# Performance work log

Measured on AMD Instinct MI355X. Metric: run time of the kernel, lower is better.

The kernel has to match this reference:

```python
import jax, jax.numpy as jnp
import numpy as np

COS_EPS = 1e-8  # torch F.cosine_similarity eps


def setup_inputs() -> dict:
    key = jax.random.key(0)
    k1, k2 = jax.random.split(key)
    x = jax.random.normal(k1, (8192, 512), dtype=jnp.float32)
    class_logits = jax.random.normal(k2, (8192, 100), dtype=jnp.float32)
    return {"x": x, "class_logits": class_logits}


def reference(x, class_logits):
    N, D = x.shape
    C = class_logits.shape[1]

    # class_logits.clone().detach()
    logits = jax.lax.stop_gradient(class_logits)
    pred = jax.nn.softmax(logits, axis=1)
    max_logit = pred.max(axis=1)          # [N]
    max_cls = pred.argmax(axis=1)         # [N] int

    # graph(): pairwise cosine similarity = normalize rows + gram matmul
    norms = jnp.linalg.norm(x, axis=1, keepdims=True)
    xn = x / jnp.maximum(norms, COS_EPS)
    mat = xn @ xn.T                       # [N, N]

    x_agg = mat @ x + x                   # [N, D]
    x_new = jax.lax.stop_gradient(x_agg)

    # update_prototype: per-class weighted scatter-add then mean over counts
    weighted = x_new * max_logit[:, None]                     # [N, D]
    sums = jax.ops.segment_sum(weighted, max_cls, num_segments=C)      # [C, D]
    counts = jax.ops.segment_sum(jnp.ones((N,), x.dtype), max_cls, num_segments=C)  # [C]
    prototypes = jnp.where(counts[:, None] > 0,
                           sums / jnp.maximum(counts, 1.0)[:, None],
                           jnp.zeros_like(sums))              # [C, D]

    # inter_class_matrix[i, j] = prototypes[j] - prototypes[i]
    inter_class_matrix = prototypes[None, :, :] - prototypes[:, None, :]  # [C, C, D]
    return prototypes, inter_class_matrix
```

## Files before the change

### kernel.cpp

```cpp
#include <hip/hip_runtime.h>
#include <math.h>

#define N_ROWS 8192
#define D_DIM  512
#define C_CLS  100

typedef unsigned short u16;
typedef __attribute__((ext_vector_type(8))) short short8;
typedef __attribute__((ext_vector_type(4))) float floatx4;

#define WS_G      0
#define WS_SUMS   262144
#define WS_COUNTS 313344
#define WS_INV    313472
#define WS_WV     321664
#define WS_CLS    329856
#define WS_GH     338048
#define WS_GL     469120
#define WS_XH     600192
#define WS_XL     2697344
#define WS_XTH    4794496
#define WS_XTL    6891648
#define WS_NTH    8988800
#define WS_NTL    11085952
#define WS_ZERO_FLOATS 313472

__device__ __forceinline__ void split2(float v, u16& h, u16& l) {
    unsigned u = __float_as_uint(v);
    h = (u16)(u >> 16);
    float r = v - __uint_as_float(u & 0xFFFF0000u);
    l = (u16)(__float_as_uint(r) >> 16);
}

__global__ void k_softmax(const float* __restrict__ logits,
                          float* __restrict__ wv, int* __restrict__ cls,
                          float* __restrict__ counts) {
    int wave = (blockIdx.x * blockDim.x + threadIdx.x) >> 6;
    int lane = threadIdx.x & 63;
    if (wave >= N_ROWS) return;
    const float* row = logits + (size_t)wave * C_CLS;
    float v1 = row[lane];
    bool has2 = (lane + 64) < C_CLS;
    float v2 = has2 ? row[lane + 64] : -INFINITY;
    float m; int idx;
    if (v2 > v1) { m = v2; idx = lane + 64; } else { m = v1; idx = lane; }
    #pragma unroll
    for (int off = 32; off >= 1; off >>= 1) {
        float om = __shfl_down(m, off);
        int   oi = __shfl_down(idx, off);
        if (om > m || (om == m && oi < idx)) { m = om; idx = oi; }
    }
    m = __shfl(m, 0);
    idx = __shfl(idx, 0);
    float s = expf(v1 - m) + (has2 ? expf(v2 - m) : 0.0f);
    #pragma unroll
    for (int off = 32; off >= 1; off >>= 1) s += __shfl_down(s, off);
    if (lane == 0) {
        wv[wave] = 1.0f / s;
        cls[wave] = idx;
        atomicAdd(&counts[idx], 1.0f);
    }
}

__global__ void k_norm(const float* __restrict__ x, float* __restrict__ inv) {
    int wave = (blockIdx.x * blockDim.x + threadIdx.x) >> 6;
    int lane = threadIdx.x & 63;
    if (wave >= N_ROWS) return;
    const float* row = x + (size_t)wave * D_DIM;
    float ss = 0.f;
    #pragma unroll
    for (int j = 0; j < D_DIM; j += 64) {
        float v = row[j + lane];
        ss += v * v;
    }
    #pragma unroll
    for (int off = 32; off >= 1; off >>= 1) ss += __shfl_down(ss, off);
    if (lane == 0) inv[wave] = 1.0f / fmaxf(sqrtf(ss), 1e-8f);
}

#define LDT 65
__global__ __launch_bounds__(256) void k_convert(const float* __restrict__ x,
        const float* __restrict__ inv,
        u16* __restrict__ xh, u16* __restrict__ xl,
        u16* __restrict__ xth, u16* __restrict__ xtl,
        u16* __restrict__ nth, u16* __restrict__ ntl) {
    __shared__ unsigned xt_p[64 * LDT];
    __shared__ unsigned nt_p[64 * LDT];
    int r0 = blockIdx.x * 64, c0 = blockIdx.y * 64;
    int t = threadIdx.x;
    int r = t >> 2, cq = t & 3;
    const float* src = x + (size_t)(r0 + r) * D_DIM + c0 + cq * 16;
    float vv[16];
    {
        float4 a = *(const float4*)(src + 0);
        float4 b = *(const float4*)(src + 4);
        float4 c = *(const float4*)(src + 8);
        float4 d = *(const float4*)(src + 12);
        vv[0]=a.x; vv[1]=a.y; vv[2]=a.z; vv[3]=a.w;
        vv[4]=b.x; vv[5]=b.y; vv[6]=b.z; vv[7]=b.w;
        vv[8]=c.x; vv[9]=c.y; vv[10]=c.z; vv[11]=c.w;
        vv[12]=d.x; vv[13]=d.y; vv[14]=d.z; vv[15]=d.w;
    }
    float iv = inv[r0 + r];
    u16 hh[16], ll[16];
    #pragma unroll
    for (int j = 0; j < 16; ++j) {
        split2(vv[j], hh[j], ll[j]);
        u16 nh, nl;
        split2(iv * vv[j], nh, nl);
        int cl = cq * 16 + j;
        xt_p[cl * LDT + r] = ((unsigned)hh[j] << 16) | ll[j];
        nt_p[cl * LDT + r] = ((unsigned)nh   << 16) | nl;
    }
    {
        size_t base = (size_t)(r0 + r) * D_DIM + c0 + cq * 16;
        uint oh[8], ol[8];
        #pragma unroll
        for (int p = 0; p < 8; ++p) {
            oh[p] = (unsigned)hh[2*p] | ((unsigned)hh[2*p+1] << 16);
            ol[p] = (unsigned)ll[2*p] | ((unsigned)ll[2*p+1] << 16);
        }
        *(uint4*)&xh[base]     = make_uint4(oh[0], oh[1], oh[2], oh[3]);
        *(uint4*)&xh[base + 8] = make_uint4(oh[4], oh[5], oh[6], oh[7]);
        *(uint4*)&xl[base]     = make_uint4(ol[0], ol[1], ol[2], ol[3]);
        *(uint4*)&xl[base + 8] = make_uint4(ol[4], ol[5], ol[6], ol[7]);
    }
    __syncthreads();
    int c = t >> 2, rq = (t & 3) * 16;
    size_t tbase = (size_t)(c0 + c) * N_ROWS + r0 + rq;
    {
        uint oh[8], ol[8];
        #pragma unroll
        for (int p = 0; p < 8; ++p) {
            unsigned d0 = xt_p[c * LDT + rq + 2*p];
            unsigned d1 = xt_p[c * LDT + rq + 2*p + 1];
            oh[p] = (d0 >> 16) | (d1 & 0xFFFF0000u);
            ol[p] = (d0 & 0xFFFFu) | (d1 << 16);
        }
        *(uint4*)&xth[tbase]     = make_uint4(oh[0], oh[1], oh[2], oh[3]);
        *(uint4*)&xth[tbase + 8] = make_uint4(oh[4], oh[5], oh[6], oh[7]);
        *(uint4*)&xtl[tbase]     = make_uint4(ol[0], ol[1], ol[2], ol[3]);
        *(uint4*)&xtl[tbase + 8] = make_uint4(ol[4], ol[5], ol[6], ol[7]);
    }
    {
        uint oh[8], ol[8];
        #pragma unroll
        for (int p = 0; p < 8; ++p) {
            unsigned d0 = nt_p[c * LDT + rq + 2*p];
            unsigned d1 = nt_p[c * LDT + rq + 2*p + 1];
            oh[p] = (d0 >> 16) | (d1 & 0xFFFF0000u);
            ol[p] = (d0 & 0xFFFFu) | (d1 << 16);
        }
        *(uint4*)&nth[tbase]     = make_uint4(oh[0], oh[1], oh[2], oh[3]);
        *(uint4*)&nth[tbase + 8] = make_uint4(oh[4], oh[5], oh[6], oh[7]);
        *(uint4*)&ntl[tbase]     = make_uint4(ol[0], ol[1], ol[2], ol[3]);
        *(uint4*)&ntl[tbase + 8] = make_uint4(ol[4], ol[5], ol[6], ol[7]);
    }
}

#define STR 40
__global__ __launch_bounds__(256) void k_gemm1(const u16* __restrict__ nth,
        const u16* __restrict__ ntl, const u16* __restrict__ xth,
        const u16* __restrict__ xtl, float* __restrict__ G) {
    __shared__ u16 Ah[64 * STR], Al[64 * STR], Bh[64 * STR], Bl[64 * STR];
    int i0 = (blockIdx.x & 7) * 64, j0 = (blockIdx.x >> 3) * 64;
    int kb = blockIdx.y * (N_ROWS / 8);
    int t = threadIdx.x, w = t >> 6, l = t & 63;
    int sr = t >> 2, sc = (t & 3) * 8;
    floatx4 acc[4];
    floatx4 zero = {0.f, 0.f, 0.f, 0.f};
    #pragma unroll
    for (int nn = 0; nn < 4; ++nn) acc[nn] = zero;
    for (int s = 0; s < 32; ++s) {
        int ks = kb + s * 32 + sc;
        *(uint4*)&Ah[sr * STR + sc] = *(const uint4*)&nth[(size_t)(i0 + sr) * N_ROWS + ks];
        *(uint4*)&Al[sr * STR + sc] = *(const uint4*)&ntl[(size_t)(i0 + sr) * N_ROWS + ks];
        *(uint4*)&Bh[sr * STR + sc] = *(const uint4*)&xth[(size_t)(j0 + sr) * N_ROWS + ks];
        *(uint4*)&Bl[sr * STR + sc] = *(const uint4*)&xtl[(size_t)(j0 + sr) * N_ROWS + ks];
        __syncthreads();
        int ar = (w * 16 + (l & 15)) * STR + (l >> 4) * 8;
        short8 a_h = *(const short8*)&Ah[ar];
        short8 a_l = *(const short8*)&Al[ar];
        #pragma unroll
        for (int nn = 0; nn < 4; ++nn) {
            int br = (nn * 16 + (l & 15)) * STR + (l >> 4) * 8;
            short8 b_h = *(const short8*)&Bh[br];
            short8 b_l = *(const short8*)&Bl[br];
            acc[nn] = __builtin_amdgcn_mfma_f32_16x16x32_bf16(a_h, b_h, acc[nn], 0, 0, 0);
            acc[nn] = __builtin_amdgcn_mfma_f32_16x16x32_bf16(a_h, b_l, acc[nn], 0, 0, 0);
            acc[nn] = __builtin_amdgcn_mfma_f32_16x16x32_bf16(a_l, b_h, acc[nn], 0, 0, 0);
        }
        __syncthreads();
    }
    int row0 = i0 + w * 16 + (l >> 4) * 4;
    int col0 = j0 + (l & 15);
    #pragma unroll
    for (int nn = 0; nn < 4; ++nn)
        #pragma unroll
        for (int r = 0; r < 4; ++r)
            atomicAdd(&G[(size_t)(row0 + r) * D_DIM + col0 + nn * 16], acc[nn][r]);
}

__global__ void k_split(const float* __restrict__ G, u16* __restrict__ Gh,
                        u16* __restrict__ Gl) {
    int i = blockIdx.x * 256 + threadIdx.x;
    u16 h, l;
    split2(G[i], h, l);
    Gh[i] = h; Gl[i] = l;
}

__global__ __launch_bounds__(256) void k_gemm2(const u16* __restrict__ xh,
        const u16* __restrict__ xl, const u16* __restrict__ Gh,
        const u16* __restrict__ Gl, const float* __restrict__ x,
        const float* __restrict__ inv, const float* __restrict__ wv,
        const int* __restrict__ cls, float* __restrict__ sums) {
    __shared__ u16 Xh[128 * STR], Xl[128 * STR], Bh2[64 * STR], Bl2[64 * STR];
    int m0 = blockIdx.x * 128, j0 = blockIdx.y * 64;
    int t = threadIdx.x, w = t >> 6, l = t & 63;
    int sr = t >> 2, sc = (t & 3) * 8;
    floatx4 acc[2][4];
    floatx4 zero = {0.f, 0.f, 0.f, 0.f};
    #pragma unroll
    for (int mi = 0; mi < 2; ++mi)
        #pragma unroll
        for (int nn = 0; nn < 4; ++nn) acc[mi][nn] = zero;
    for (int s = 0; s < 16; ++s) {
        int ks = s * 32 + sc;
        *(uint4*)&Xh[sr * STR + sc]        = *(const uint4*)&xh[(size_t)(m0 + sr) * D_DIM + ks];
        *(uint4*)&Xh[(64 + sr) * STR + sc] = *(const uint4*)&xh[(size_t)(m0 + 64 + sr) * D_DIM + ks];
        *(uint4*)&Xl[sr * STR + sc]        = *(const uint4*)&xl[(size_t)(m0 + sr) * D_DIM + ks];
        *(uint4*)&Xl[(64 + sr) * STR + sc] = *(const uint4*)&xl[(size_t)(m0 + 64 + sr) * D_DIM + ks];
        *(uint4*)&Bh2[sr * STR + sc]       = *(const uint4*)&Gh[(size_t)(j0 + sr) * D_DIM + ks];
        *(uint4*)&Bl2[sr * STR + sc]       = *(const uint4*)&Gl[(size_t)(j0 + sr) * D_DIM + ks];
        __syncthreads();
        int ar0 = (w * 32 + (l & 15)) * STR + (l >> 4) * 8;
        int ar1 = (w * 32 + 16 + (l & 15)) * STR + (l >> 4) * 8;
        short8 ah0 = *(const short8*)&Xh[ar0];
        short8 al0 = *(const short8*)&Xl[ar0];
        short8 ah1 = *(const short8*)&Xh[ar1];
        short8 al1 = *(const short8*)&Xl[ar1];
        #pragma unroll
        for (int nn = 0; nn < 4; ++nn) {
            int br = (nn * 16 + (l & 15)) * STR + (l >> 4) * 8;
            short8 b_h = *(const short8*)&Bh2[br];
            short8 b_l = *(const short8*)&Bl2[br];
            acc[0][nn] = __builtin_amdgcn_mfma_f32_16x16x32_bf16(ah0, b_h, acc[0][nn], 0, 0, 0);
            acc[0][nn] = __builtin_amdgcn_mfma_f32_16x16x32_bf16(ah0, b_l, acc[0][nn], 0, 0, 0);
            acc[0][nn] = __builtin_amdgcn_mfma_f32_16x16x32_bf16(al0, b_h, acc[0][nn], 0, 0, 0);
            acc[1][nn] = __builtin_amdgcn_mfma_f32_16x16x32_bf16(ah1, b_h, acc[1][nn], 0, 0, 0);
            acc[1][nn] = __builtin_amdgcn_mfma_f32_16x16x32_bf16(ah1, b_l, acc[1][nn], 0, 0, 0);
            acc[1][nn] = __builtin_amdgcn_mfma_f32_16x16x32_bf16(al1, b_h, acc[1][nn], 0, 0, 0);
        }
        __syncthreads();
    }
    int col = j0 + (l & 15);
    #pragma unroll
    for (int mi = 0; mi < 2; ++mi) {
        int rb = m0 + w * 32 + mi * 16 + (l >> 4) * 4;
        #pragma unroll
        for (int r = 0; r < 4; ++r) {
            int m = rb + r;
            float ivm = inv[m], wm = wv[m];
            int cm = cls[m];
            #pragma unroll
            for (int nn = 0; nn < 4; ++nn) {
                int d = col + nn * 16;
                float y = ivm * acc[mi][nn][r] + x[(size_t)m * D_DIM + d];
                atomicAdd(&sums[(size_t)cm * D_DIM + d], wm * y);
            }
        }
    }
}

__global__ void k_proto(const float* __restrict__ sums,
                        const float* __restrict__ counts,
                        float* __restrict__ out) {
    int i = blockIdx.x * blockDim.x + threadIdx.x;
    if (i >= C_CLS * D_DIM) return;
    int c = i >> 9;
    float cnt = counts[c];
    out[i] = (cnt > 0.f) ? sums[i] / fmaxf(cnt, 1.f) : 0.f;
}

__global__ void k_inter(const float* __restrict__ proto, float* __restrict__ out) {
    int pair = blockIdx.x;
    int i = pair / C_CLS;
    int j = pair - i * C_CLS;
    int d = threadIdx.x << 2;
    float4 pj = *(const float4*)&proto[j * D_DIM + d];
    float4 pi = *(const float4*)&proto[i * D_DIM + d];
    float4 r;
    r.x = pj.x - pi.x; r.y = pj.y - pi.y; r.z = pj.z - pi.z; r.w = pj.w - pi.w;
    *(float4*)&out[(size_t)pair * D_DIM + d] = r;
}

extern "C" void kernel_launch(void* const* d_in, const int* in_sizes, int n_in,
                              void* d_out, int out_size, void* d_ws, size_t ws_size,
                              hipStream_t stream) {
    const float* x      = (const float*)d_in[0];
    const float* logits = (const float*)d_in[1];
    float* out = (float*)d_out;
    float* ws  = (float*)d_ws;
    float* G      = ws + WS_G;
    float* sums   = ws + WS_SUMS;
    float* counts = ws + WS_COUNTS;
    float* inv    = ws + WS_INV;
    float* wv     = ws + WS_WV;
    int*   cls    = (int*)(ws + WS_CLS);
    u16* Gh  = (u16*)(ws + WS_GH);
    u16* Gl  = (u16*)(ws + WS_GL);
    u16* xh  = (u16*)(ws + WS_XH);
    u16* xl  = (u16*)(ws + WS_XL);
    u16* xth = (u16*)(ws + WS_XTH);
    u16* xtl = (u16*)(ws + WS_XTL);
    u16* nth = (u16*)(ws + WS_NTH);
    u16* ntl = (u16*)(ws + WS_NTL);

    hipMemsetAsync(d_ws, 0, WS_ZERO_FLOATS * sizeof(float), stream);
    k_softmax<<<N_ROWS / 4, 256, 0, stream>>>(logits, wv, cls, counts);
    k_norm<<<N_ROWS / 4, 256, 0, stream>>>(x, inv);
    k_convert<<<dim3(128, 8), 256, 0, stream>>>(x, inv, xh, xl, xth, xtl, nth, ntl);
    k_gemm1<<<dim3(64, 8), 256, 0, stream>>>(nth, ntl, xth, xtl, G);
    k_split<<<D_DIM * D_DIM / 256, 256, 0, stream>>>(G, Gh, Gl);
    k_gemm2<<<dim3(64, 8), 256, 0, stream>>>(xh, xl, Gh, Gl, x, inv, wv, cls, sums);
    k_proto<<<(C_CLS * D_DIM + 255) / 256, 256, 0, stream>>>(sums, counts, out);
    k_inter<<<C_CLS * C_CLS, 128, 0, stream>>>(out, out + C_CLS * D_DIM);
}
```

Baseline: 195.6 us.

## Reassociate prototype computation to per-class reductions times Gram matrix, drop second GEMM

The N×D by D×D second GEMM and its atomic scatter are replaced by an algebraic reassociation. Rows are bucketed by class through a count, scan and scatter pass. Each class then reduces its weighted rows into two D-vectors and multiplies one of them by the D×D Gram matrix G in fp32. The first GEMM now uses 128x128 tiles with global_load_lds direct copies and writes 32 K-split partials, which a separate kernel reduces instead of using float atomics. This removes the large second GEMM, the x split buffers and the G split step. In exchange it adds extra small kernels, a 32 MB partial buffer, and a per-class loop whose length depends on how many rows land in each class.

```diff
diff --git a/kernel.cpp b/kernel.cpp
--- a/kernel.cpp
+++ b/kernel.cpp
@@ -6,24 +6,23 @@
 #define C_CLS  100
 
 typedef unsigned short u16;
+typedef unsigned int u32;
 typedef __attribute__((ext_vector_type(8))) short short8;
 typedef __attribute__((ext_vector_type(4))) float floatx4;
 
 #define WS_G      0
-#define WS_SUMS   262144
-#define WS_COUNTS 313344
-#define WS_INV    313472
-#define WS_WV     321664
-#define WS_CLS    329856
-#define WS_GH     338048
-#define WS_GL     469120
-#define WS_XH     600192
-#define WS_XL     2697344
-#define WS_XTH    4794496
-#define WS_XTL    6891648
-#define WS_NTH    8988800
-#define WS_NTL    11085952
-#define WS_ZERO_FLOATS 313472
+#define WS_GP     262144
+#define WS_INV    8650752
+#define WS_WV     8658944
+#define WS_CLS    8667136
+#define WS_CNT    8675328
+#define WS_OFFS   8675456
+#define WS_CUR    8675584
+#define WS_ORDER  8675712
+#define WS_NTH    8683904
+#define WS_NTL    10781056
+#define WS_XTH    12878208
+#define WS_XTL    14975360
 
 __device__ __forceinline__ void split2(float v, u16& h, u16& l) {
     unsigned u = __float_as_uint(v);
@@ -32,9 +31,15 @@
     l = (u16)(__float_as_uint(r) >> 16);
 }
 
+typedef const __attribute__((address_space(1))) u32* gp32;
+typedef __attribute__((address_space(3))) u32* lp32;
+__device__ __forceinline__ void cp16(const u16* g, u16* l) {
+    __builtin_amdgcn_global_load_lds((gp32)g, (lp32)l, 16, 0, 0);
+}
+
 __global__ void k_softmax(const float* __restrict__ logits,
                           float* __restrict__ wv, int* __restrict__ cls,
-                          float* __restrict__ counts) {
+                          int* __restrict__ cnt) {
     int wave = (blockIdx.x * blockDim.x + threadIdx.x) >> 6;
     int lane = threadIdx.x & 63;
     if (wave >= N_ROWS) return;
@@ -58,7 +63,7 @@
     if (lane == 0) {
         wv[wave] = 1.0f / s;
         cls[wave] = idx;
-        atomicAdd(&counts[idx], 1.0f);
+        atomicAdd(&cnt[idx], 1);
     }
 }
 
@@ -78,10 +83,24 @@
     if (lane == 0) inv[wave] = 1.0f / fmaxf(sqrtf(ss), 1e-8f);
 }
 
+__global__ void k_scan(const int* __restrict__ cnt, int* __restrict__ offs) {
+    if (threadIdx.x == 0) {
+        int acc = 0;
+        for (int c = 0; c < C_CLS; ++c) { offs[c] = acc; acc += cnt[c]; }
+    }
+}
+
+__global__ void k_scatter(const int* __restrict__ cls, const int* __restrict__ offs,
+                          int* __restrict__ cursor, int* __restrict__ order) {
+    int m = blockIdx.x * 256 + threadIdx.x;
+    int c = cls[m];
+    int pos = atomicAdd(&cursor[c], 1);
+    order[offs[c] + pos] = m;
+}
+
 #define LDT 65
 __global__ __launch_bounds__(256) void k_convert(const float* __restrict__ x,
         const float* __restrict__ inv,
-        u16* __restrict__ xh, u16* __restrict__ xl,
         u16* __restrict__ xth, u16* __restrict__ xtl,
         u16* __restrict__ nth, u16* __restrict__ ntl) {
     __shared__ unsigned xt_p[64 * LDT];
@@ -102,28 +121,14 @@
         vv[12]=d.x; vv[13]=d.y; vv[14]=d.z; vv[15]=d.w;
     }
     float iv = inv[r0 + r];
-    u16 hh[16], ll[16];
     #pragma unroll
     for (int j = 0; j < 16; ++j) {
-        split2(vv[j], hh[j], ll[j]);
-        u16 nh, nl;
+        u16 h, l, nh, nl;
+        split2(vv[j], h, l);
         split2(iv * vv[j], nh, nl);
         int cl = cq * 16 + j;
-        xt_p[cl * LDT + r] = ((unsigned)hh[j] << 16) | ll[j];
-        nt_p[cl * LDT + r] = ((unsigned)nh   << 16) | nl;
-    }
-    {
-        size_t base = (size_t)(r0 + r) * D_DIM + c0 + cq * 16;
-        uint oh[8], ol[8];
-        #pragma unroll
-        for (int p = 0; p < 8; ++p) {
-            oh[p] = (unsigned)hh[2*p] | ((unsigned)hh[2*p+1] << 16);
-            ol[p] = (unsigned)ll[2*p] | ((unsigned)ll[2*p+1] << 16);
-        }
-        *(uint4*)&xh[base]     = make_uint4(oh[0], oh[1], oh[2], oh[3]);
-        *(uint4*)&xh[base + 8] = make_uint4(oh[4], oh[5], oh[6], oh[7]);
-        *(uint4*)&xl[base]     = make_uint4(ol[0], ol[1], ol[2], ol[3]);
-        *(uint4*)&xl[base + 8] = make_uint4(ol[4], ol[5], ol[6], ol[7]);
+        xt_p[cl * LDT + r] = ((unsigned)h  << 16) | l;
+        nt_p[cl * LDT + r] = ((unsigned)nh << 16) | nl;
     }
     __syncthreads();
     int c = t >> 2, rq = (t & 3) * 16;
@@ -158,128 +163,114 @@
     }
 }
 
-#define STR 40
-__global__ __launch_bounds__(256) void k_gemm1(const u16* __restrict__ nth,
+__global__ __launch_bounds__(256, 2) void k_gemm1(const u16* __restrict__ nth,
         const u16* __restrict__ ntl, const u16* __restrict__ xth,
-        const u16* __restrict__ xtl, float* __restrict__ G) {
-    __shared__ u16 Ah[64 * STR], Al[64 * STR], Bh[64 * STR], Bl[64 * STR];
-    int i0 = (blockIdx.x & 7) * 64, j0 = (blockIdx.x >> 3) * 64;
-    int kb = blockIdx.y * (N_ROWS / 8);
+        const u16* __restrict__ xtl, float* __restrict__ Gp) {
+    __shared__ __attribute__((aligned(16))) u16 Ah[128*32], Al[128*32];
+    __shared__ __attribute__((aligned(16))) u16 Bh[128*32], Bl[128*32];
+    int i0 = (blockIdx.x & 3) << 7, j0 = (blockIdx.x >> 2) << 7;
+    int kb = blockIdx.y << 8;
     int t = threadIdx.x, w = t >> 6, l = t & 63;
-    int sr = t >> 2, sc = (t & 3) * 8;
-    floatx4 acc[4];
-    floatx4 zero = {0.f, 0.f, 0.f, 0.f};
-    #pragma unroll
-    for (int nn = 0; nn < 4; ++nn) acc[nn] = zero;
-    for (int s = 0; s < 32; ++s) {
-        int ks = kb + s * 32 + sc;
-        *(uint4*)&Ah[sr * STR + sc] = *(const uint4*)&nth[(size_t)(i0 + sr) * N_ROWS + ks];
-        *(uint4*)&Al[sr * STR + sc] = *(const uint4*)&ntl[(size_t)(i0 + sr) * N_ROWS + ks];
-        *(uint4*)&Bh[sr * STR + sc] = *(const uint4*)&xth[(size_t)(j0 + sr) * N_ROWS + ks];
-        *(uint4*)&Bl[sr * STR + sc] = *(const uint4*)&xtl[(size_t)(j0 + sr) * N_ROWS + ks];
+    int srow = t >> 2, scol = (t & 3) << 3;
+    int lm = l & 15, lg = l >> 4;
+    floatx4 acc[4][4];
+    #pragma unroll
+    for (int mi = 0; mi < 4; ++mi)
+        #pragma unroll
+        for (int ni = 0; ni < 4; ++ni) acc[mi][ni] = (floatx4){0.f,0.f,0.f,0.f};
+    int d0 = srow * 32 + scol;
+    int d1 = (64 + srow) * 32 + scol;
+    const size_t ga0 = (size_t)(i0 + srow) * N_ROWS + kb + scol;
+    const size_t ga1 = (size_t)(i0 + 64 + srow) * N_ROWS + kb + scol;
+    const size_t gb0 = (size_t)(j0 + srow) * N_ROWS + kb + scol;
+    const size_t gb1 = (size_t)(j0 + 64 + srow) * N_ROWS + kb + scol;
+    for (int s = 0; s < 8; ++s) {
+        int ks = s << 5;
+        cp16(nth + ga0 + ks, Ah + d0);
+        cp16(nth + ga1 + ks, Ah + d1);
+        cp16(ntl + ga0 + ks, Al + d0);
+        cp16(ntl + ga1 + ks, Al + d1);
+        cp16(xth + gb0 + ks, Bh + d0);
+        cp16(xth + gb1 + ks, Bh + d1);
+        cp16(xtl + gb0 + ks, Bl + d0);
+        cp16(xtl + gb1 + ks, Bl + d1);
         __syncthreads();
-        int ar = (w * 16 + (l & 15)) * STR + (l >> 4) * 8;
-        short8 a_h = *(const short8*)&Ah[ar];
-        short8 a_l = *(const short8*)&Al[ar];
-        #pragma unroll
-        for (int nn = 0; nn < 4; ++nn) {
-            int br = (nn * 16 + (l & 15)) * STR + (l >> 4) * 8;
-            short8 b_h = *(const short8*)&Bh[br];
-            short8 b_l = *(const short8*)&Bl[br];
-            acc[nn] = __builtin_amdgcn_mfma_f32_16x16x32_bf16(a_h, b_h, acc[nn], 0, 0, 0);
-            acc[nn] = __builtin_amdgcn_mfma_f32_16x16x32_bf16(a_h, b_l, acc[nn], 0, 0, 0);
-            acc[nn] = __builtin_amdgcn_mfma_f32_16x16x32_bf16(a_l, b_h, acc[nn], 0, 0, 0);
-        }
+        short8 ah[4], al[4], bh[4], bl[4];
+        #pragma unroll
+        for (int mi = 0; mi < 4; ++mi) {
+            int off = (((w & 1) << 6) + (mi << 4) + lm) * 32 + (lg << 3);
+            ah[mi] = *(const short8*)&Ah[off];
+            al[mi] = *(const short8*)&Al[off];
+        }
+        #pragma unroll
+        for (int ni = 0; ni < 4; ++ni) {
+            int off = (((w >> 1) << 6) + (ni << 4) + lm) * 32 + (lg << 3);
+            bh[ni] = *(const short8*)&Bh[off];
+            bl[ni] = *(const short8*)&Bl[off];
+        }
+        #pragma unroll
+        for (int mi = 0; mi < 4; ++mi)
+            #pragma unroll
+            for (int ni = 0; ni < 4; ++ni) {
+                acc[mi][ni] = __builtin_amdgcn_mfma_f32_16x16x32_bf16(ah[mi], bh[ni], acc[mi][ni], 0, 0, 0);
+                acc[mi][ni] = __builtin_amdgcn_mfma_f32_16x16x32_bf16(ah[mi], bl[ni], acc[mi][ni], 0, 0, 0);
+                acc[mi][ni] = __builtin_amdgcn_mfma_f32_16x16x32_bf16(al[mi], bh[ni], acc[mi][ni], 0, 0, 0);
+            }
         __syncthreads();
     }
-    int row0 = i0 + w * 16 + (l >> 4) * 4;
-    int col0 = j0 + (l & 15);
-    #pragma unroll
-    for (int nn = 0; nn < 4; ++nn)
-        #pragma unroll
-        for (int r = 0; r < 4; ++r)
-            atomicAdd(&G[(size_t)(row0 + r) * D_DIM + col0 + nn * 16], acc[nn][r]);
-}
-
-__global__ void k_split(const float* __restrict__ G, u16* __restrict__ Gh,
-                        u16* __restrict__ Gl) {
+    float* Gb = Gp + ((size_t)blockIdx.y << 18);
+    #pragma unroll
+    for (int mi = 0; mi < 4; ++mi) {
+        int row0 = i0 + ((w & 1) << 6) + (mi << 4) + (lg << 2);
+        #pragma unroll
+        for (int ni = 0; ni < 4; ++ni) {
+            int col = j0 + ((w >> 1) << 6) + (ni << 4) + lm;
+            #pragma unroll
+            for (int r = 0; r < 4; ++r)
+                Gb[(size_t)(row0 + r) * D_DIM + col] = acc[mi][ni][r];
+        }
+    }
+}
+
+__global__ void k_reduceG(const float* __restrict__ Gp, float* __restrict__ G) {
     int i = blockIdx.x * 256 + threadIdx.x;
-    u16 h, l;
-    split2(G[i], h, l);
-    Gh[i] = h; Gl[i] = l;
-}
-
-__global__ __launch_bounds__(256) void k_gemm2(const u16* __restrict__ xh,
-        const u16* __restrict__ xl, const u16* __restrict__ Gh,
-        const u16* __restrict__ Gl, const float* __restrict__ x,
+    float s = 0.f;
+    #pragma unroll
+    for (int p = 0; p < 32; ++p) s += Gp[(size_t)p * (D_DIM * D_DIM) + i];
+    G[i] = s;
+}
+
+__global__ __launch_bounds__(256) void k_protos(const float* __restrict__ x,
         const float* __restrict__ inv, const float* __restrict__ wv,
-        const int* __restrict__ cls, float* __restrict__ sums) {
-    __shared__ u16 Xh[128 * STR], Xl[128 * STR], Bh2[64 * STR], Bl2[64 * STR];
-    int m0 = blockIdx.x * 128, j0 = blockIdx.y * 64;
-    int t = threadIdx.x, w = t >> 6, l = t & 63;
-    int sr = t >> 2, sc = (t & 3) * 8;
-    floatx4 acc[2][4];
-    floatx4 zero = {0.f, 0.f, 0.f, 0.f};
-    #pragma unroll
-    for (int mi = 0; mi < 2; ++mi)
-        #pragma unroll
-        for (int nn = 0; nn < 4; ++nn) acc[mi][nn] = zero;
-    for (int s = 0; s < 16; ++s) {
-        int ks = s * 32 + sc;
-        *(uint4*)&Xh[sr * STR + sc]        = *(const uint4*)&xh[(size_t)(m0 + sr) * D_DIM + ks];
-        *(uint4*)&Xh[(64 + sr) * STR + sc] = *(const uint4*)&xh[(size_t)(m0 + 64 + sr) * D_DIM + ks];
-        *(uint4*)&Xl[sr * STR + sc]        = *(const uint4*)&xl[(size_t)(m0 + sr) * D_DIM + ks];
-        *(uint4*)&Xl[(64 + sr) * STR + sc] = *(const uint4*)&xl[(size_t)(m0 + 64 + sr) * D_DIM + ks];
-        *(uint4*)&Bh2[sr * STR + sc]       = *(const uint4*)&Gh[(size_t)(j0 + sr) * D_DIM + ks];
-        *(uint4*)&Bl2[sr * STR + sc]       = *(const uint4*)&Gl[(size_t)(j0 + sr) * D_DIM + ks];
-        __syncthreads();
-        int ar0 = (w * 32 + (l & 15)) * STR + (l >> 4) * 8;
-        int ar1 = (w * 32 + 16 + (l & 15)) * STR + (l >> 4) * 8;
-        short8 ah0 = *(const short8*)&Xh[ar0];
-        short8 al0 = *(const short8*)&Xl[ar0];
-        short8 ah1 = *(const short8*)&Xh[ar1];
-        short8 al1 = *(const short8*)&Xl[ar1];
-        #pragma unroll
-        for (int nn = 0; nn < 4; ++nn) {
-            int br = (nn * 16 + (l & 15)) * STR + (l >> 4) * 8;
-            short8 b_h = *(const short8*)&Bh2[br];
-            short8 b_l = *(const short8*)&Bl2[br];
-            acc[0][nn] = __builtin_amdgcn_mfma_f32_16x16x32_bf16(ah0, b_h, acc[0][nn], 0, 0, 0);
-            acc[0][nn] = __builtin_amdgcn_mfma_f32_16x16x32_bf16(ah0, b_l, acc[0][nn], 0, 0, 0);
-            acc[0][nn] = __builtin_amdgcn_mfma_f32_16x16x32_bf16(al0, b_h, acc[0][nn], 0, 0, 0);
-            acc[1][nn] = __builtin_amdgcn_mfma_f32_16x16x32_bf16(ah1, b_h, acc[1][nn], 0, 0, 0);
-            acc[1][nn] = __builtin_amdgcn_mfma_f32_16x16x32_bf16(ah1, b_l, acc[1][nn], 0, 0, 0);
-            acc[1][nn] = __builtin_amdgcn_mfma_f32_16x16x32_bf16(al1, b_h, acc[1][nn], 0, 0, 0);
-        }
-        __syncthreads();
-    }
-    int col = j0 + (l & 15);
-    #pragma unroll
-    for (int mi = 0; mi < 2; ++mi) {
-        int rb = m0 + w * 32 + mi * 16 + (l >> 4) * 4;
-        #pragma unroll
-        for (int r = 0; r < 4; ++r) {
-            int m = rb + r;
-            float ivm = inv[m], wm = wv[m];
-            int cm = cls[m];
-            #pragma unroll
-            for (int nn = 0; nn < 4; ++nn) {
-                int d = col + nn * 16;
-                float y = ivm * acc[mi][nn][r] + x[(size_t)m * D_DIM + d];
-                atomicAdd(&sums[(size_t)cm * D_DIM + d], wm * y);
-            }
-        }
-    }
-}
-
-__global__ void k_proto(const float* __restrict__ sums,
-                        const float* __restrict__ counts,
-                        float* __restrict__ out) {
-    int i = blockIdx.x * blockDim.x + threadIdx.x;
-    if (i >= C_CLS * D_DIM) return;
-    int c = i >> 9;
-    float cnt = counts[c];
-    out[i] = (cnt > 0.f) ? sums[i] / fmaxf(cnt, 1.f) : 0.f;
+        const int* __restrict__ order, const int* __restrict__ offs,
+        const int* __restrict__ cnt, const float* __restrict__ G,
+        float* __restrict__ out) {
+    __shared__ float u_s[D_DIM];
+    int c = blockIdx.x;
+    int t = threadIdx.x;
+    int n = cnt[c], o = offs[c];
+    float u0 = 0.f, u1 = 0.f, v0 = 0.f, v1 = 0.f;
+    for (int p = 0; p < n; ++p) {
+        int m = order[o + p];
+        float wm = wv[m];
+        float wi = wm * inv[m];
+        float xa = x[(size_t)m * D_DIM + t];
+        float xb = x[(size_t)m * D_DIM + t + 256];
+        u0 += wi * xa; u1 += wi * xb;
+        v0 += wm * xa; v1 += wm * xb;
+    }
+    u_s[t] = u0; u_s[t + 256] = u1;
+    __syncthreads();
+    float a0 = v0, a1 = v1;
+    for (int k = 0; k < D_DIM; ++k) {
+        float uk = u_s[k];
+        const float* Gr = G + (size_t)k * D_DIM;
+        a0 += uk * Gr[t];
+        a1 += uk * Gr[t + 256];
+    }
+    float s = (n > 0) ? 1.0f / (float)n : 0.0f;
+    out[(size_t)c * D_DIM + t]       = a0 * s;
+    out[(size_t)c * D_DIM + t + 256] = a1 * s;
 }
 
 __global__ void k_inter(const float* __restrict__ proto, float* __restrict__ out) {
@@ -301,28 +292,28 @@
     const float* logits = (const float*)d_in[1];
     float* out = (float*)d_out;
     float* ws  = (float*)d_ws;
-    float* G      = ws + WS_G;
-    float* sums   = ws + WS_SUMS;
-    float* counts = ws + WS_COUNTS;
-    float* inv    = ws + WS_INV;
-    float* wv     = ws + WS_WV;
-    int*   cls    = (int*)(ws + WS_CLS);
-    u16* Gh  = (u16*)(ws + WS_GH);
-    u16* Gl  = (u16*)(ws + WS_GL);
-    u16* xh  = (u16*)(ws + WS_XH);
-    u16* xl  = (u16*)(ws + WS_XL);
+    float* G     = ws + WS_G;
+    float* Gp    = ws + WS_GP;
+    float* inv   = ws + WS_INV;
+    float* wv    = ws + WS_WV;
+    int*   cls   = (int*)(ws + WS_CLS);
+    int*   cnt   = (int*)(ws + WS_CNT);
+    int*   offs  = (int*)(ws + WS_OFFS);
+    int*   cur   = (int*)(ws + WS_CUR);
+    int*   order = (int*)(ws + WS_ORDER);
+    u16* nth = (u16*)(ws + WS_NTH);
+    u16* ntl = (u16*)(ws + WS_NTL);
     u16* xth = (u16*)(ws + WS_XTH);
     u16* xtl = (u16*)(ws + WS_XTL);
-    u16* nth = (u16*)(ws + WS_NTH);
-    u16* ntl = (u16*)(ws + WS_NTL);
-
-    hipMemsetAsync(d_ws, 0, WS_ZERO_FLOATS * sizeof(float), stream);
-    k_softmax<<<N_ROWS / 4, 256, 0, stream>>>(logits, wv, cls, counts);
+
+    hipMemsetAsync((void*)cnt, 0, 384 * sizeof(int), stream);
+    k_softmax<<<N_ROWS / 4, 256, 0, stream>>>(logits, wv, cls, cnt);
     k_norm<<<N_ROWS / 4, 256, 0, stream>>>(x, inv);
-    k_convert<<<dim3(128, 8), 256, 0, stream>>>(x, inv, xh, xl, xth, xtl, nth, ntl);
-    k_gemm1<<<dim3(64, 8), 256, 0, stream>>>(nth, ntl, xth, xtl, G);
-    k_split<<<D_DIM * D_DIM / 256, 256, 0, stream>>>(G, Gh, Gl);
-    k_gemm2<<<dim3(64, 8), 256, 0, stream>>>(xh, xl, Gh, Gl, x, inv, wv, cls, sums);
-    k_proto<<<(C_CLS * D_DIM + 255) / 256, 256, 0, stream>>>(sums, counts, out);
+    k_scan<<<1, 64, 0, stream>>>(cnt, offs);
+    k_scatter<<<N_ROWS / 256, 256, 0, stream>>>(cls, offs, cur, order);
+    k_convert<<<dim3(128, 8), 256, 0, stream>>>(x, inv, xth, xtl, nth, ntl);
+    k_gemm1<<<dim3(16, 32), 256, 0, stream>>>(nth, ntl, xth, xtl, Gp);
+    k_reduceG<<<D_DIM * D_DIM / 256, 256, 0, stream>>>(Gp, G);
+    k_protos<<<C_CLS, 256, 0, stream>>>(x, inv, wv, order, offs, cnt, G, out);
     k_inter<<<C_CLS * C_CLS, 128, 0, stream>>>(out, out + C_CLS * D_DIM);
 }
```

Measured after the change: 206.0 us. +5.3%, slower.
